# Optimization experiments

Hardware: AMD Instinct MI355X
Metric: run time of the kernel (lower is better)

Reference implementation:

```python
import jax, jax.numpy as jnp
import numpy as np

INPUT_SIZE = 512
HIDDEN_SIZE = 1024
SEQ_LEN = 512
BATCH = 64

def _xavier(key, shape):
    fan_out, fan_in = shape
    bound = float(np.sqrt(6.0 / (fan_in + fan_out)))
    return jax.random.uniform(key, shape, jnp.float32, -bound, bound)

def setup_inputs() -> dict:
    key = jax.random.key(0)
    ks = jax.random.split(key, 5)
    return {
        "x_seq": jax.random.normal(ks[0], (SEQ_LEN, BATCH, INPUT_SIZE), jnp.float32),
        "h0": jax.random.normal(ks[1], (BATCH, HIDDEN_SIZE), jnp.float32),
        "U_c": _xavier(ks[2], (HIDDEN_SIZE, INPUT_SIZE)),
        "w_c": jnp.ones((HIDDEN_SIZE,), jnp.float32),
        "b_c": jnp.zeros((HIDDEN_SIZE,), jnp.float32),
        "U_a": _xavier(ks[3], (HIDDEN_SIZE, INPUT_SIZE)),
        "w_a": jnp.ones((HIDDEN_SIZE,), jnp.float32),
        "b_a": jnp.zeros((HIDDEN_SIZE,), jnp.float32),
        "U_h": _xavier(ks[4], (HIDDEN_SIZE, INPUT_SIZE)),
        "b_h": jnp.zeros((HIDDEN_SIZE,), jnp.float32),
    }

def reference(x_seq, h0, U_c, w_c, b_c, U_a, w_a, b_a, U_h, b_h):
    # Batch the three input projections across all timesteps (the compute-heavy
    # GEMMs), then run the inherently-sequential gated recurrence with lax.scan.
    xc = jnp.einsum('tbi,hi->tbh', x_seq, U_c) + b_c  # [T, B, H]
    xa = jnp.einsum('tbi,hi->tbh', x_seq, U_a) + b_a
    xh = jnp.einsum('tbi,hi->tbh', x_seq, U_h) + b_h

    def step(h, proj):
        pc, pa, ph = proj
        c = jax.nn.sigmoid(pc + w_c * h)
        a = 1.0 + jnp.tanh(pa + w_a * h)
        h_new = c * h + (1.0 - c) * jnp.tanh(ph + a * h)
        return h_new, h_new

    h_last, y_seq = jax.lax.scan(step, h0, (xc, xa, xh))
    return (y_seq, (h_last,))
```

## Files before the change

### kernel.cpp

```cpp
#include <hip/hip_runtime.h>
#include <cstdint>
#include <cstddef>

#define T_SEQ 512
#define BATCH 64
#define IN_SZ 512
#define HID   1024
#define BH    (BATCH*HID)
#define M_TOT (T_SEQ*BATCH)
#define D_CH  16

typedef float f32x4 __attribute__((ext_vector_type(4)));
typedef _Float16 f16x8 __attribute__((ext_vector_type(8)));

__device__ inline unsigned short f2h(float f){
  union { _Float16 h; unsigned short u; } v;
  v.h = (_Float16)f;
  return v.u;
}
__device__ inline float h2f(unsigned short s){
  union { unsigned short u; _Float16 h; } v; v.u = s;
  return (float)v.h;
}

__device__ inline float sigm_f(float x){ return 1.f/(1.f + __expf(-x)); }
__device__ inline float tanh_f(float x){ float e = __expf(2.f*x); return 1.f - 2.f/(e + 1.f); }

__device__ inline void async16(const void* g, void* l){
  __builtin_amdgcn_global_load_lds(
      (__attribute__((address_space(1))) void*)g,
      (__attribute__((address_space(3))) void*)l,
      16, 0, 0);
}

__global__ __launch_bounds__(256) void cvt_all(
    const float* __restrict__ x,  const float* __restrict__ Uc,
    const float* __restrict__ Ua, const float* __restrict__ Uh,
    unsigned short* __restrict__ xb, unsigned short* __restrict__ U0,
    unsigned short* __restrict__ U1, unsigned short* __restrict__ U2)
{
  const int b = blockIdx.x, t = threadIdx.x;
  if (b < 1024){
    const int i0 = b*256 + t;
#pragma unroll
    for (int k = 0; k < 16; ++k){
      const int i = i0 + k*262144;
      float4 v = ((const float4*)x)[i];
      ushort4 o;
      o.x = f2h(v.x); o.y = f2h(v.y); o.z = f2h(v.z); o.w = f2h(v.w);
      ((ushort4*)xb)[i] = o;
    }
  } else {
    const int i = (b - 1024)*256 + t;
    {
      float4 v = ((const float4*)Uc)[i];
      ushort4 o; o.x=f2h(v.x); o.y=f2h(v.y); o.z=f2h(v.z); o.w=f2h(v.w);
      ((ushort4*)U0)[i] = o;
    }
    {
      float4 v = ((const float4*)Ua)[i];
      ushort4 o; o.x=f2h(v.x); o.y=f2h(v.y); o.z=f2h(v.z); o.w=f2h(v.w);
      ((ushort4*)U1)[i] = o;
    }
    {
      float4 v = ((const float4*)Uh)[i];
      ushort4 o; o.x=f2h(v.x); o.y=f2h(v.y); o.z=f2h(v.z); o.w=f2h(v.w);
      ((ushort4*)U2)[i] = o;
    }
  }
}

__global__ __launch_bounds__(512, 2) void gemm3(
    const unsigned short* __restrict__ xb,
    const unsigned short* __restrict__ U0,
    const unsigned short* __restrict__ U1,
    const unsigned short* __restrict__ U2,
    const float* __restrict__ b0, const float* __restrict__ b1, const float* __restrict__ b2,
    unsigned short* out0, unsigned short* out1, void* out2, int ph_f16)
{
  __shared__ __align__(16) unsigned char smem_raw[131072];

  const int tid  = threadIdx.x;
  const int wave = tid >> 6, lane = tid & 63;
  const int quad = lane >> 4, l16 = lane & 15;

  const int bid  = blockIdx.x;
  const int xcd  = bid & 7;
  const int slot = bid >> 3;
  const int mbl  = slot / 12;
  const int inner= slot - mbl*12;
  const int mb   = xcd*16 + mbl;
  const int z    = inner % 3;
  const int nb   = inner / 3;

  const int m0 = mb * 256, n0 = nb * 256;
  const unsigned short* Um = (z==0) ? U0 : (z==1) ? U1 : U2;
  const float* bias        = (z==0) ? b0 : (z==1) ? b1 : b2;
  const int wm = wave >> 2, wn = wave & 3;

  const int laneRow = lane >> 2;
  const int cg8     = ((lane & 3) ^ ((lane >> 3) & 3)) << 3;
  const unsigned short* srcA = xb + (size_t)m0 * IN_SZ;
  const unsigned short* srcB = Um + (size_t)n0 * IN_SZ;

  const int cxa = l16*64 + ((quad ^ ((l16 >> 1) & 3)) << 4);

  auto stageA = [&](int tile, int kh){
    unsigned char* dst = smem_raw + (((tile & 1)*2 + kh) << 14);
#pragma unroll
    for (int j = 0; j < 2; ++j){
      const unsigned short* g = srcA + (size_t)((wave*2 + j)*16 + laneRow)*IN_SZ
                                + tile*64 + kh*32 + cg8;
      async16(g, dst + (wave*2 + j)*1024);
    }
  };
  auto stageB = [&](int tile, int kh){
    unsigned char* dst = smem_raw + 65536 + (((tile & 1)*2 + kh) << 14);
#pragma unroll
    for (int j = 0; j < 2; ++j){
      const unsigned short* g = srcB + (size_t)((wave*2 + j)*16 + laneRow)*IN_SZ
                                + tile*64 + kh*32 + cg8;
      async16(g, dst + (wave*2 + j)*1024);
    }
  };

  const f32x4 zf = {0.f, 0.f, 0.f, 0.f};
  f32x4 acc[8][4];
#pragma unroll
  for (int i = 0; i < 8; ++i)
#pragma unroll
    for (int j = 0; j < 4; ++j) acc[i][j] = zf;

  stageA(0,0); stageB(0,0); stageA(0,1); stageB(0,1);
  stageA(1,0); stageB(1,0); stageA(1,1);
  asm volatile("s_waitcnt vmcnt(10)" ::: "memory");
  __builtin_amdgcn_s_barrier();

#define CLUSTER(B0_, B1_, N0_, N1_)                                                      \
  __builtin_amdgcn_s_barrier();                                                          \
  asm volatile("s_waitcnt lgkmcnt(0)" ::: "memory");                                     \
  __builtin_amdgcn_s_setprio(1);                                                         \
  _Pragma("unroll")                                                                      \
  for (int im_ = 0; im_ < 8; ++im_){                                                     \
    acc[im_][N0_] = __builtin_amdgcn_mfma_f32_16x16x32_f16(a0[im_], B0_, acc[im_][N0_], 0,0,0); \
    acc[im_][N1_] = __builtin_amdgcn_mfma_f32_16x16x32_f16(a0[im_], B1_, acc[im_][N1_], 0,0,0); \
  }                                                                                      \
  __builtin_amdgcn_s_setprio(0);                                                         \
  __builtin_amdgcn_s_barrier();

  f16x8 a0[8];
#pragma unroll
  for (int g = 0; g < 8; ++g){
    const int buf = g & 1;
    const unsigned char* Ab0 = smem_raw + ((buf*2 + 0) << 14);
    const unsigned char* Ab1 = smem_raw + ((buf*2 + 1) << 14);
    const unsigned char* Bb0 = smem_raw + 65536 + ((buf*2 + 0) << 14);
    const unsigned char* Bb1 = smem_raw + 65536 + ((buf*2 + 1) << 14);

#pragma unroll
    for (int im = 0; im < 8; ++im)
      a0[im] = *(const f16x8*)(Ab0 + wm*8192 + im*1024 + cxa);
    f16x8 q0 = *(const f16x8*)(Bb0 + wn*4096 + 0*1024 + cxa);
    f16x8 q1 = *(const f16x8*)(Bb0 + wn*4096 + 1*1024 + cxa);
    if (g < 7) stageB(g+1, 1);
    CLUSTER(q0, q1, 0, 1)

    f16x8 q2 = *(const f16x8*)(Bb0 + wn*4096 + 2*1024 + cxa);
    f16x8 q3 = *(const f16x8*)(Bb0 + wn*4096 + 3*1024 + cxa);
    if (g < 6) stageA(g+2, 0);
    if (g < 6)      { asm volatile("s_waitcnt vmcnt(10)" ::: "memory"); }
    else if (g == 6){ asm volatile("s_waitcnt vmcnt(8)"  ::: "memory"); }
    else            { asm volatile("s_waitcnt vmcnt(0)"  ::: "memory"); }
    CLUSTER(q2, q3, 2, 3)

#pragma unroll
    for (int im = 0; im < 8; ++im)
      a0[im] = *(const f16x8*)(Ab1 + wm*8192 + im*1024 + cxa);
    q0 = *(const f16x8*)(Bb1 + wn*4096 + 0*1024 + cxa);
    q1 = *(const f16x8*)(Bb1 + wn*4096 + 1*1024 + cxa);
    if (g < 6) stageB(g+2, 0);
    CLUSTER(q0, q1, 0, 1)

    q2 = *(const f16x8*)(Bb1 + wn*4096 + 2*1024 + cxa);
    q3 = *(const f16x8*)(Bb1 + wn*4096 + 3*1024 + cxa);
    if (g < 6) stageA(g+2, 1);
    if (g < 6)      { asm volatile("s_waitcnt vmcnt(10)" ::: "memory"); }
    else if (g == 6){ asm volatile("s_waitcnt vmcnt(4)"  ::: "memory"); }
    CLUSTER(q2, q3, 2, 3)
  }
#undef CLUSTER

  float bv[4];
#pragma unroll
  for (int in = 0; in < 4; ++in) bv[in] = bias[n0 + wn*64 + in*16 + l16];

  if (z == 2 && !ph_f16) {
    float* o32 = (float*)out2;
#pragma unroll
    for (int im = 0; im < 8; ++im)
#pragma unroll
      for (int r = 0; r < 4; ++r){
        int grow = m0 + wm*128 + im*16 + quad*4 + r;
        size_t rb = (size_t)grow * HID;
#pragma unroll
        for (int in = 0; in < 4; ++in)
          o32[rb + n0 + wn*64 + in*16 + l16] = acc[im][in][r] + bv[in];
      }
    return;
  }

  unsigned short* op = (z==0) ? out0 : (z==1) ? out1 : (unsigned short*)out2;
  unsigned short* sw = (unsigned short*)smem_raw + wave*4608;
#pragma unroll
  for (int h = 0; h < 2; ++h){
#pragma unroll
    for (int i4 = 0; i4 < 4; ++i4){
      int im = h*4 + i4;
#pragma unroll
      for (int r = 0; r < 4; ++r){
        int lr = i4*16 + quad*4 + r;
#pragma unroll
        for (int in = 0; in < 4; ++in)
          sw[lr*72 + in*16 + l16] = f2h(acc[im][in][r] + bv[in]);
      }
    }
    asm volatile("s_waitcnt lgkmcnt(0)" ::: "memory");
#pragma unroll
    for (int i = 0; i < 8; ++i){
      int lr = i*8 + (lane >> 3);
      int ch = lane & 7;
      uint4 v = *(const uint4*)(sw + lr*72 + ch*8);
      int grow = m0 + wm*128 + h*64 + lr;
      *(uint4*)(op + (size_t)grow*HID + n0 + wn*64 + ch*8) = v;
    }
    if (h == 0) asm volatile("s_waitcnt lgkmcnt(0)" ::: "memory");
  }
}

template <bool PH16>
__global__ __launch_bounds__(256) void scan_k(
    const unsigned short* __restrict__ pc, const unsigned short* __restrict__ pa,
    const void* __restrict__ phv,
    float* __restrict__ y,
    const float* __restrict__ h0, const float* __restrict__ wc, const float* __restrict__ wa,
    float* __restrict__ hlast)
{
  __shared__ __align__(16) unsigned char sm[65536];
  const int tid  = threadIdx.x;
  const int wave = tid >> 6, lane = tid & 63;
  const int col0 = blockIdx.x * 256;
  const int idx  = col0 + tid;
  const int hidx = idx & (HID - 1);

  float h = h0[idx];
  const float wcv = wc[hidx], wav = wa[hidx];
  const unsigned short* ph16 = (const unsigned short*)phv;
  const float*          ph32 = (const float*)phv;

  unsigned char* pcL = sm;
  unsigned char* paL = sm + 16384;
  unsigned char* phL = sm + 32768;

  auto stage = [&](int c){
    const int b  = c & 1;
    const int t0 = c * D_CH;
#pragma unroll
    for (int j = 0; j < 2; ++j){
      const int tr  = wave*2 + j*8;
      const int row = tr + (lane >> 5);
      const int ce  = (lane & 31) * 8;
      async16(pc + (size_t)(t0+row)*BH + col0 + ce, pcL + b*8192 + tr*512);
      async16(pa + (size_t)(t0+row)*BH + col0 + ce, paL + b*8192 + tr*512);
    }
    if (PH16){
#pragma unroll
      for (int j = 0; j < 2; ++j){
        const int tr  = wave*2 + j*8;
        const int row = tr + (lane >> 5);
        const int ce  = (lane & 31) * 8;
        async16(ph16 + (size_t)(t0+row)*BH + col0 + ce, phL + b*8192 + tr*512);
      }
    } else {
#pragma unroll
      for (int j = 0; j < 4; ++j){
        const int t = wave + j*4;
        async16(ph32 + (size_t)(t0+t)*BH + col0 + lane*4, phL + b*16384 + t*1024);
      }
    }
  };

  stage(0);
  asm volatile("s_waitcnt vmcnt(0)" ::: "memory");
  __builtin_amdgcn_s_barrier();
  __builtin_amdgcn_sched_barrier(0);

  constexpr int NC = T_SEQ / D_CH;
  for (int c = 0; c < NC; ++c){
    if (c + 1 < NC) stage(c + 1);
    const int b  = c & 1;
    const int t0 = c * D_CH;
    const unsigned short* pcb   = (const unsigned short*)(pcL + b*8192)  + tid;
    const unsigned short* pab   = (const unsigned short*)(paL + b*8192)  + tid;
    const unsigned short* phb16 = (const unsigned short*)(phL + b*8192)  + tid;
    const float*          phb32 = (const float*)(phL + b*16384) + tid;
#pragma unroll
    for (int i = 0; i < D_CH; ++i){
      float pcv = h2f(pcb[i*256]);
      float pav = h2f(pab[i*256]);
      float ph_ = PH16 ? h2f(phb16[i*256]) : phb32[i*256];
      float cc = sigm_f(pcv + wcv*h);
      float a  = 1.f + tanh_f(pav + wav*h);
      float hc = tanh_f(ph_ + a*h);
      h = cc*h + (1.f - cc)*hc;
      y[(size_t)(t0 + i)*BH + idx] = h;
    }
    if (c + 1 < NC){
      asm volatile("s_waitcnt vmcnt(16)" ::: "memory");
      __builtin_amdgcn_s_barrier();
      __builtin_amdgcn_sched_barrier(0);
    }
  }
  hlast[idx] = h;
}

extern "C" void kernel_launch(void* const* d_in, const int* in_sizes, int n_in,
                              void* d_out, int out_size, void* d_ws, size_t ws_size,
                              hipStream_t stream)
{
  const float* x  = (const float*)d_in[0];
  const float* h0 = (const float*)d_in[1];
  const float* Uc = (const float*)d_in[2];
  const float* wc = (const float*)d_in[3];
  const float* bc = (const float*)d_in[4];
  const float* Ua = (const float*)d_in[5];
  const float* wa = (const float*)d_in[6];
  const float* ba = (const float*)d_in[7];
  const float* Uh = (const float*)d_in[8];
  const float* bh = (const float*)d_in[9];

  float* y     = (float*)d_out;
  float* hlast = y + (size_t)T_SEQ * BH;

  const size_t szP16 = (size_t)T_SEQ * BH * 2;
  const size_t szX16 = (size_t)M_TOT * IN_SZ * 2;
  const size_t szU16 = (size_t)HID * IN_SZ * 2;

  const size_t base = 2*szP16 + szX16 + 3*szU16;
  const bool ph_sep = ws_size >= base + szP16;

  char* w = (char*)d_ws;
  unsigned short* pc16 = (unsigned short*)w;
  unsigned short* pa16 = (unsigned short*)(w + szP16);
  unsigned short* xb   = (unsigned short*)(w + 2*szP16);
  unsigned short* U0b  = (unsigned short*)(w + 2*szP16 + szX16);
  unsigned short* U1b  = U0b + szU16/2;
  unsigned short* U2b  = U1b + szU16/2;
  unsigned short* ph16 = (unsigned short*)(w + base);

  cvt_all<<<1536, 256, 0, stream>>>(x, Uc, Ua, Uh, xb, U0b, U1b, U2b);

  void* phbuf = ph_sep ? (void*)ph16 : (void*)y;
  gemm3<<<1536, 512, 0, stream>>>(xb, U0b, U1b, U2b, bc, ba, bh,
                                  pc16, pa16, phbuf, ph_sep ? 1 : 0);

  if (ph_sep)
    scan_k<true><<<BH/256, 256, 0, stream>>>(pc16, pa16, (const void*)ph16,
                                             y, h0, wc, wa, hlast);
  else
    scan_k<false><<<BH/256, 256, 0, stream>>>(pc16, pa16, (const void*)y,
                                              y, h0, wc, wa, hlast);
}
```

Measured before the change: 397.9 us.

## Give each wave private LDS staging to drop block barriers in recurrence

Each wave now async-loads only the 64 columns it consumes into its own LDS region, instead of the block cooperatively staging 256 columns. This removes the per-chunk s_barrier, so waves wait only on their own vmcnt and never stall on slower waves. The waitcnt thresholds are recounted to cover the stores issued in between. The risks are a wrong vmcnt count and narrower 128-byte row segments per load, which may lower coalescing efficiency.

```diff
diff --git a/kernel.cpp b/kernel.cpp
--- a/kernel.cpp
+++ b/kernel.cpp
@@ -257,67 +257,72 @@
   const unsigned short* ph16 = (const unsigned short*)phv;
   const float*          ph32 = (const float*)phv;
 
-  unsigned char* pcL = sm;
-  unsigned char* paL = sm + 16384;
-  unsigned char* phL = sm + 32768;
+  unsigned char* wr  = sm + wave*16384;
+  unsigned char* pcW = wr;
+  unsigned char* paW = wr + 4096;
+  unsigned char* phW = wr + 8192;
+
+  const int colW = col0 + wave*64;
+  const int r8   = lane >> 3;
+  const int c8   = (lane & 7) * 8;
+  const int r4   = lane >> 4;
+  const int c4   = (lane & 15) * 4;
 
   auto stage = [&](int c){
     const int b  = c & 1;
     const int t0 = c * D_CH;
 #pragma unroll
     for (int j = 0; j < 2; ++j){
-      const int tr  = wave*2 + j*8;
-      const int row = tr + (lane >> 5);
-      const int ce  = (lane & 31) * 8;
-      async16(pc + (size_t)(t0+row)*BH + col0 + ce, pcL + b*8192 + tr*512);
-      async16(pa + (size_t)(t0+row)*BH + col0 + ce, paL + b*8192 + tr*512);
+      const int row = t0 + j*8 + r8;
+      async16(pc + (size_t)row*BH + colW + c8, pcW + b*2048 + j*1024);
+      async16(pa + (size_t)row*BH + colW + c8, paW + b*2048 + j*1024);
     }
     if (PH16){
 #pragma unroll
       for (int j = 0; j < 2; ++j){
-        const int tr  = wave*2 + j*8;
-        const int row = tr + (lane >> 5);
-        const int ce  = (lane & 31) * 8;
-        async16(ph16 + (size_t)(t0+row)*BH + col0 + ce, phL + b*8192 + tr*512);
+        const int row = t0 + j*8 + r8;
+        async16(ph16 + (size_t)row*BH + colW + c8, phW + b*2048 + j*1024);
       }
     } else {
 #pragma unroll
       for (int j = 0; j < 4; ++j){
-        const int t = wave + j*4;
-        async16(ph32 + (size_t)(t0+t)*BH + col0 + lane*4, phL + b*16384 + t*1024);
+        const int row = t0 + j*4 + r4;
+        async16(ph32 + (size_t)row*BH + colW + c4, phW + b*4096 + j*1024);
       }
     }
   };
 
+  constexpr int NC = T_SEQ / D_CH;
   stage(0);
-  asm volatile("s_waitcnt vmcnt(0)" ::: "memory");
-  __builtin_amdgcn_s_barrier();
-  __builtin_amdgcn_sched_barrier(0);
-
-  constexpr int NC = T_SEQ / D_CH;
   for (int c = 0; c < NC; ++c){
     if (c + 1 < NC) stage(c + 1);
+    if (c == 0){
+      if (PH16) asm volatile("s_waitcnt vmcnt(6)"  ::: "memory");
+      else      asm volatile("s_waitcnt vmcnt(8)"  ::: "memory");
+    } else if (c + 1 < NC){
+      if (PH16) asm volatile("s_waitcnt vmcnt(22)" ::: "memory");
+      else      asm volatile("s_waitcnt vmcnt(24)" ::: "memory");
+    } else {
+      asm volatile("s_waitcnt vmcnt(16)" ::: "memory");
+    }
+    __builtin_amdgcn_sched_barrier(0);
+
     const int b  = c & 1;
     const int t0 = c * D_CH;
-    const unsigned short* pcb   = (const unsigned short*)(pcL + b*8192)  + tid;
-    const unsigned short* pab   = (const unsigned short*)(paL + b*8192)  + tid;
-    const unsigned short* phb16 = (const unsigned short*)(phL + b*8192)  + tid;
-    const float*          phb32 = (const float*)(phL + b*16384) + tid;
+    const unsigned char* pcb = pcW + b*2048 + lane*2;
+    const unsigned char* pab = paW + b*2048 + lane*2;
+    const unsigned char* phb = phW + (PH16 ? b*2048 + lane*2 : b*4096 + lane*4);
 #pragma unroll
     for (int i = 0; i < D_CH; ++i){
-      float pcv = h2f(pcb[i*256]);
-      float pav = h2f(pab[i*256]);
-      float ph_ = PH16 ? h2f(phb16[i*256]) : phb32[i*256];
+      float pcv = h2f(*(const unsigned short*)(pcb + i*128));
+      float pav = h2f(*(const unsigned short*)(pab + i*128));
+      float ph_ = PH16 ? h2f(*(const unsigned short*)(phb + i*128))
+                       : *(const float*)(phb + i*256);
       float cc = sigm_f(pcv + wcv*h);
       float a  = 1.f + tanh_f(pav + wav*h);
       float hc = tanh_f(ph_ + a*h);
       h = cc*h + (1.f - cc)*hc;
       y[(size_t)(t0 + i)*BH + idx] = h;
-    }
-    if (c + 1 < NC){
-      asm volatile("s_waitcnt vmcnt(16)" ::: "memory");
-      __builtin_amdgcn_s_barrier();
-      __builtin_amdgcn_sched_barrier(0);
     }
   }
   hlast[idx] = h;
```

Measured after the change: 372.9 us. 6.3% less time.
